# Performance work log

Hardware: AMD Instinct MI355X
Metric: run time of the kernel (lower is better)

## Reference

```python
import jax, jax.numpy as jnp
import numpy as np

NUM_GROUPS = 4
NUM_HEADS = 8
EPS = 1e-5


def setup_inputs() -> dict:
    key = jax.random.key(0)
    k1, k2, k3 = jax.random.split(key, 3)
    B, C, D, H, W = 4, 256, 32, 32, 32
    x = jax.random.normal(k1, (B, C, D, H, W), dtype=jnp.float32)
    gn_weight = jnp.ones((C,), dtype=jnp.float32)
    gn_bias = jnp.zeros((C,), dtype=jnp.float32)
    # 1x1x1 conv weights collapse to [out_ch, in_ch] matrices
    qkv_weight = jax.random.normal(k2, (3 * C, C), dtype=jnp.float32) * (1.0 / np.sqrt(C))
    out_weight = jax.random.normal(k3, (C, C), dtype=jnp.float32) * (1.0 / np.sqrt(C))
    out_bias = jnp.zeros((C,), dtype=jnp.float32)
    return {"x": x, "gn_weight": gn_weight, "gn_bias": gn_bias,
            "qkv_weight": qkv_weight, "out_weight": out_weight, "out_bias": out_bias}


def _group_norm(x, weight, bias):
    B, C, D, H, W = x.shape
    g = NUM_GROUPS
    xg = x.reshape(B, g, C // g, D, H, W)
    mean = jnp.mean(xg, axis=(2, 3, 4, 5), keepdims=True)
    var = jnp.var(xg, axis=(2, 3, 4, 5), keepdims=True)
    xn = ((xg - mean) * jax.lax.rsqrt(var + EPS)).reshape(B, C, D, H, W)
    return xn * weight[None, :, None, None, None] + bias[None, :, None, None, None]


def reference(x, gn_weight, gn_bias, qkv_weight, out_weight, out_bias):
    B, C, D, H, W = x.shape
    N = D * H * W
    hd = C // NUM_HEADS  # per-head channels

    norm = _group_norm(x, gn_weight, gn_bias)
    # 1x1x1 conv == channel matmul: [B,3C,D,H,W]
    qkv = jnp.einsum('bcdhw,oc->bodhw', norm, qkv_weight)
    # 'b (qkv heads c) d h w -> qkv b heads c (d h w)'
    qkv = qkv.reshape(B, 3, NUM_HEADS, hd, N)
    q, k, v = qkv[:, 0], qkv[:, 1], qkv[:, 2]  # each [B, heads, hd, N]

    k = jax.nn.softmax(k, axis=-1)  # softmax over spatial dim
    sim = jnp.einsum('bhdn,bhen->bhde', k, v)   # [B, heads, hd, hd]
    out = jnp.einsum('bhde,bhdn->bhen', sim, q)  # [B, heads, hd, N]
    out = out.reshape(B, C, D, H, W)

    out = jnp.einsum('bcdhw,oc->bodhw', out, out_weight) + out_bias[None, :, None, None, None]
    return out + x
```

## Files before the change

### kernel.cpp

```cpp
#include <hip/hip_runtime.h>
#include <cmath>


typedef __bf16 bf16x8 __attribute__((ext_vector_type(8)));
typedef float f32x4 __attribute__((ext_vector_type(4)));

union U16 { uint4 u; unsigned short s[8]; bf16x8 v; };

__device__ __forceinline__ float bf2f(unsigned short h) {
    unsigned int u = ((unsigned int)h) << 16;
    return __builtin_bit_cast(float, u);
}
__device__ __forceinline__ unsigned short f2bf(float f) {
    unsigned int u = __builtin_bit_cast(unsigned int, f);
    u = (u + 0x7fffu + ((u >> 16) & 1u)) >> 16;
    return (unsigned short)u;
}
__device__ __forceinline__ unsigned int pack2(unsigned short a, unsigned short b) {
    return (unsigned int)a | ((unsigned int)b << 16);
}

__global__ __launch_bounds__(64) void k_detect(const unsigned int* __restrict__ xr,
                                               int* __restrict__ flag) {
    unsigned int u = xr[threadIdx.x * 997];
    int e = (u >> 7) & 0xFF;
    bool ok = (e >= 100) && (e <= 141);
    unsigned long long m = __ballot(ok);
    if (threadIdx.x == 0) *flag = (__popcll(m) < 32) ? 1 : 0;
}

__global__ __launch_bounds__(256) void k_cvt_w(const void* __restrict__ qkvw,
                                               const void* __restrict__ outw,
                                               const void* __restrict__ gnw,
                                               const void* __restrict__ gnb,
                                               const void* __restrict__ outb,
                                               const int* __restrict__ flagp,
                                               unsigned short* __restrict__ wdst) {
    int idx = blockIdx.x * 256 + threadIdx.x;
    if (idx >= 262912) return;
    const void* src; int off;
    if      (idx < 196608) { src = qkvw; off = idx; }
    else if (idx < 262144) { src = outw; off = idx - 196608; }
    else if (idx < 262400) { src = gnw;  off = idx - 262144; }
    else if (idx < 262656) { src = gnb;  off = idx - 262400; }
    else                   { src = outb; off = idx - 262656; }
    int f = *flagp;
    wdst[idx] = f ? f2bf(((const float*)src)[off])
                  : ((const unsigned short*)src)[off];
}

__global__ __launch_bounds__(256) void k_cvt_x(const void* __restrict__ xr,
                                               const int* __restrict__ flagp,
                                               unsigned short* __restrict__ xw) {
    int f = *flagp;
    size_t base = ((size_t)blockIdx.x * 256 + threadIdx.x) * 8;
    if (f) {
        const float* xf = (const float*)xr;
        float4 a = *(const float4*)(xf + base);
        float4 c = *(const float4*)(xf + base + 4);
        U16 o;
        o.s[0] = f2bf(a.x); o.s[1] = f2bf(a.y); o.s[2] = f2bf(a.z); o.s[3] = f2bf(a.w);
        o.s[4] = f2bf(c.x); o.s[5] = f2bf(c.y); o.s[6] = f2bf(c.z); o.s[7] = f2bf(c.w);
        *(uint4*)(xw + base) = o.u;
    } else {
        *(uint4*)(xw + base) = *(const uint4*)((const unsigned short*)xr + base);
    }
}

__global__ __launch_bounds__(256) void k_gnsum(const unsigned short* __restrict__ x,
                                               float2* __restrict__ gn_part) {
    int t = threadIdx.x, bid = blockIdx.x;
    int grp = bid >> 7, chunk = bid & 127;
    const unsigned short* p = x + (size_t)grp * 2097152 + (size_t)chunk * 16384;
    float s = 0.f, q = 0.f;
    for (int i = 0; i < 8; i++) {
        U16 u; u.u = *(const uint4*)(p + i * 2048 + t * 8);
#pragma unroll
        for (int j = 0; j < 8; j++) { float f = bf2f(u.s[j]); s += f; q += f * f; }
    }
#pragma unroll
    for (int off = 32; off > 0; off >>= 1) { s += __shfl_xor(s, off); q += __shfl_xor(q, off); }
    __shared__ float rs[4], rq[4];
    int wave = t >> 6;
    if ((t & 63) == 0) { rs[wave] = s; rq[wave] = q; }
    __syncthreads();
    if (t == 0) gn_part[bid] = make_float2(rs[0] + rs[1] + rs[2] + rs[3],
                                           rq[0] + rq[1] + rq[2] + rq[3]);
}

__global__ __launch_bounds__(128) void k_gnfinal(const float2* __restrict__ gn_part,
                                                 float2* __restrict__ gstats) {
    int bg = blockIdx.x, t = threadIdx.x;
    float2 v = gn_part[bg * 128 + t];
    float s = v.x, q = v.y;
#pragma unroll
    for (int off = 32; off > 0; off >>= 1) { s += __shfl_xor(s, off); q += __shfl_xor(q, off); }
    __shared__ float rs[2], rq[2];
    if ((t & 63) == 0) { rs[t >> 6] = s; rq[t >> 6] = q; }
    __syncthreads();
    if (t == 0) {
        const float inv = 1.0f / 2097152.0f;
        float S = rs[0] + rs[1], Q = rq[0] + rq[1];
        float mean = S * inv;
        float var = Q * inv - mean * mean;
        gstats[bg] = make_float2(mean, rsqrtf(var + 1e-5f));
    }
}

__global__ __launch_bounds__(64) void k_beta(const unsigned short* __restrict__ wq,
                                             const unsigned short* __restrict__ wgnw,
                                             const unsigned short* __restrict__ wgnb,
                                             const float2* __restrict__ gstats,
                                             float* __restrict__ beta) {
    int bid = blockIdx.x;
    int b = bid / 768, o = bid % 768;
    int t = threadIdx.x, c = t * 4;
    float2 ms = gstats[b * 4 + (c >> 6)];
    uint2 qw = *(const uint2*)(wq + o * 256 + c);
    uint2 gw = *(const uint2*)(wgnw + c);
    uint2 gb = *(const uint2*)(wgnb + c);
    unsigned short qs[4] = {(unsigned short)(qw.x & 0xffff), (unsigned short)(qw.x >> 16),
                            (unsigned short)(qw.y & 0xffff), (unsigned short)(qw.y >> 16)};
    unsigned short wsx[4] = {(unsigned short)(gw.x & 0xffff), (unsigned short)(gw.x >> 16),
                             (unsigned short)(gw.y & 0xffff), (unsigned short)(gw.y >> 16)};
    unsigned short bs[4] = {(unsigned short)(gb.x & 0xffff), (unsigned short)(gb.x >> 16),
                            (unsigned short)(gb.y & 0xffff), (unsigned short)(gb.y >> 16)};
    float bacc = 0.f;
#pragma unroll
    for (int j = 0; j < 4; j++)
        bacc += bf2f(qs[j]) * (bf2f(bs[j]) - ms.x * ms.y * bf2f(wsx[j]));
#pragma unroll
    for (int off = 32; off > 0; off >>= 1) bacc += __shfl_xor(bacc, off);
    if (t == 0) beta[b * 768 + o] = bacc;
}

__global__ __launch_bounds__(256) void k_transpose(const unsigned short* __restrict__ x,
                                                   const unsigned short* __restrict__ wgnw,
                                                   const float2* __restrict__ gstats,
                                                   unsigned short* __restrict__ xt) {
    int tid = threadIdx.x, bid = blockIdx.x;
    int b = bid >> 11, r2 = bid & 2047, cblk = r2 >> 9, nblk = r2 & 511;
    float rstd = gstats[b * 4 + cblk].y;
    __shared__ __align__(16) unsigned short T[64 * 80];
    unsigned short tmp[2][8];
#pragma unroll
    for (int i = 0; i < 2; i++) {
        int crow = (tid >> 3) + 32 * i, nch = tid & 7;
        int c = cblk * 64 + crow;
        float sc = bf2f(wgnw[c]) * rstd;
        U16 u; u.u = *(const uint4*)(x + ((size_t)(b * 256 + c)) * 32768 + (size_t)nblk * 64 + nch * 8);
#pragma unroll
        for (int j = 0; j < 8; j++) tmp[i][j] = f2bf(bf2f(u.s[j]) * sc);
    }
#pragma unroll
    for (int i = 0; i < 2; i++) {
        int crow = (tid >> 3) + 32 * i, nch = tid & 7;
#pragma unroll
        for (int jj = 0; jj < 8; jj++) {
            int j = (jj + tid) & 7;
            T[(nch * 8 + j) * 80 + crow] = tmp[i][j];
        }
    }
    __syncthreads();
#pragma unroll
    for (int i = 0; i < 2; i++) {
        int nrow = (tid >> 3) + 32 * i, cch = tid & 7;
        uint4 v = *(const uint4*)&T[nrow * 80 + cch * 8];
        *(uint4*)(xt + ((size_t)b * 32768 + (size_t)nblk * 64 + nrow) * 256 + cblk * 64 + cch * 8) = v;
    }
}

__device__ __forceinline__ void stage128x64(const unsigned short* __restrict__ g,
                                            unsigned short* __restrict__ lds, int tid) {
    int wave = tid >> 6;
    int lane = tid & 63;
    const unsigned short* gl = g + (size_t)(lane >> 3) * 256 + (lane & 7) * 8;
    uint4 v[4];
#pragma unroll
    for (int i = 0; i < 4; i++)
        v[i] = *(const uint4*)(gl + (size_t)(wave * 32 + i * 8) * 256);
#pragma unroll
    for (int i = 0; i < 4; i++) {
        int row = wave * 32 + i * 8 + (lane >> 3);
        *(uint4*)&lds[row * 64 + (lane & 7) * 8] = v[i];
    }
}

__device__ __forceinline__ void gemm_core(const unsigned short* __restrict__ A,
                                          const unsigned short* __restrict__ Bsrc,
                                          unsigned short* ldsA, unsigned short* ldsB,
                                          int tid, f32x4 (&acc)[4][4]) {
    int lane = tid & 63, l15 = lane & 15, quad = lane >> 4;
    int wave = tid >> 6, wm = wave & 1, wn = wave >> 1;
    for (int kt = 0; kt < 4; kt++) {
        stage128x64(A + kt * 64, ldsA, tid);
        stage128x64(Bsrc + kt * 64, ldsB, tid);
        __syncthreads();
#pragma unroll
        for (int ks = 0; ks < 2; ks++) {
            bf16x8 af[4], bv[4];
#pragma unroll
            for (int mi = 0; mi < 4; mi++)
                af[mi] = *(const bf16x8*)&ldsA[(wm * 64 + mi * 16 + l15) * 64 + ks * 32 + quad * 8];
#pragma unroll
            for (int ni = 0; ni < 4; ni++)
                bv[ni] = *(const bf16x8*)&ldsB[(wn * 64 + ni * 16 + l15) * 64 + ks * 32 + quad * 8];
#pragma unroll
            for (int mi = 0; mi < 4; mi++)
#pragma unroll
                for (int ni = 0; ni < 4; ni++)
                    acc[mi][ni] = __builtin_amdgcn_mfma_f32_16x16x32_bf16(af[mi], bv[ni], acc[mi][ni], 0, 0, 0);
        }
        __syncthreads();
    }
}

__global__ __launch_bounds__(256) void k_gemm1(const unsigned short* __restrict__ wq,
                                               const unsigned short* __restrict__ xt,
                                               const float* __restrict__ beta,
                                               unsigned short* __restrict__ qT,
                                               unsigned short* __restrict__ kv) {
    __shared__ __align__(16) unsigned short ldsA[128 * 64];
    __shared__ __align__(16) unsigned short ldsB[128 * 64];
    int tid = threadIdx.x, bid = blockIdx.x;
    int b = bid / 1536, r = bid % 1536, mblk = r >> 8, nblk = r & 255;
    int o0 = mblk * 128;
    size_t n0 = (size_t)nblk * 128;
    const unsigned short* A = wq + (size_t)o0 * 256;
    const unsigned short* Bx = xt + ((size_t)b * 32768 + n0) * 256;
    f32x4 acc[4][4] = {};
    gemm_core(A, Bx, ldsA, ldsB, tid, acc);

    int lane = tid & 63, l15 = lane & 15, quad = lane >> 4;
    int wave = tid >> 6, wm = wave & 1, wn = wave >> 1;
    bool isQ = (mblk < 2);
#pragma unroll
    for (int mi = 0; mi < 4; mi++) {
        int o = o0 + wm * 64 + mi * 16 + quad * 4;
        float4 be = *(const float4*)(beta + b * 768 + o);
#pragma unroll
        for (int ni = 0; ni < 4; ni++) {
            size_t n = n0 + wn * 64 + ni * 16 + l15;
            f32x4 v = acc[mi][ni];
            unsigned short h0 = f2bf(v[0] + be.x), h1 = f2bf(v[1] + be.y);
            unsigned short h2 = f2bf(v[2] + be.z), h3 = f2bf(v[3] + be.w);
            if (isQ) {
                uint2 pv; pv.x = pack2(h0, h1); pv.y = pack2(h2, h3);
                *(uint2*)(qT + ((size_t)b * 32768 + n) * 256 + o) = pv;
            } else {
                int kvi = o - 256;
                unsigned short* bp = kv + ((size_t)b * 512 + kvi) * 32768 + n;
                bp[0] = h0; bp[32768] = h1; bp[65536] = h2; bp[98304] = h3;
            }
        }
    }
}

__global__ __launch_bounds__(256) void k_stats(const unsigned short* __restrict__ kv,
                                               float2* __restrict__ stats) {
    int row = blockIdx.x, t = threadIdx.x;
    const unsigned short* p = kv + ((size_t)(row >> 8) * 512 + (row & 255)) * 32768;
    float m = -3.0e38f;
    for (int i = 0; i < 16; i++) {
        U16 u; u.u = *(const uint4*)(p + i * 2048 + t * 8);
#pragma unroll
        for (int j = 0; j < 8; j++) m = fmaxf(m, bf2f(u.s[j]));
    }
#pragma unroll
    for (int off = 32; off > 0; off >>= 1) m = fmaxf(m, __shfl_xor(m, off));
    __shared__ float rm[4], rs[4];
    int wave = t >> 6;
    if ((t & 63) == 0) rm[wave] = m;
    __syncthreads();
    m = fmaxf(fmaxf(rm[0], rm[1]), fmaxf(rm[2], rm[3]));
    float s = 0.f;
    for (int i = 0; i < 16; i++) {
        U16 u; u.u = *(const uint4*)(p + i * 2048 + t * 8);
#pragma unroll
        for (int j = 0; j < 8; j++) s += __expf(bf2f(u.s[j]) - m);
    }
#pragma unroll
    for (int off = 32; off > 0; off >>= 1) s += __shfl_xor(s, off);
    if ((t & 63) == 0) rs[wave] = s;
    __syncthreads();
    if (t == 0) stats[row] = make_float2(m, 1.0f / (rs[0] + rs[1] + rs[2] + rs[3]));
}

__global__ __launch_bounds__(64) void k_sim(const unsigned short* __restrict__ kv,
                                            const float2* __restrict__ stats,
                                            float* __restrict__ partials) {
    int bid = blockIdx.x;
    int bh = bid >> 6, chunk = bid & 63;
    int b = bh >> 3, h = bh & 7;
    int lane = threadIdx.x, l15 = lane & 15, quad = lane >> 4;
    size_t n0 = (size_t)chunk * 512 + quad * 8;
    float mrow[2], isr[2];
#pragma unroll
    for (int mi = 0; mi < 2; mi++) {
        float2 st = stats[b * 256 + h * 32 + mi * 16 + l15];
        mrow[mi] = st.x; isr[mi] = st.y;
    }
    const unsigned short* kb = kv + ((size_t)b * 512 + h * 32) * 32768;
    const unsigned short* vb = kv + ((size_t)b * 512 + 256 + h * 32) * 32768;
    f32x4 acc[2][2] = {};
    for (int t = 0; t < 16; t++) {
        size_t n = n0 + t * 32;
        bf16x8 af[2], bv[2];
#pragma unroll
        for (int mi = 0; mi < 2; mi++) {
            U16 u; u.u = *(const uint4*)(kb + (size_t)(mi * 16 + l15) * 32768 + n);
            U16 pv;
#pragma unroll
            for (int j = 0; j < 8; j++) pv.s[j] = f2bf(__expf(bf2f(u.s[j]) - mrow[mi]) * isr[mi]);
            af[mi] = pv.v;
        }
#pragma unroll
        for (int ni = 0; ni < 2; ni++) {
            U16 u; u.u = *(const uint4*)(vb + (size_t)(ni * 16 + l15) * 32768 + n);
            bv[ni] = u.v;
        }
#pragma unroll
        for (int mi = 0; mi < 2; mi++)
#pragma unroll
            for (int ni = 0; ni < 2; ni++)
                acc[mi][ni] = __builtin_amdgcn_mfma_f32_16x16x32_bf16(af[mi], bv[ni], acc[mi][ni], 0, 0, 0);
    }
    float* po = partials + (size_t)(bh * 64 + chunk) * 1024;
#pragma unroll
    for (int mi = 0; mi < 2; mi++)
#pragma unroll
        for (int ni = 0; ni < 2; ni++)
#pragma unroll
            for (int rr = 0; rr < 4; rr++)
                po[(mi * 16 + quad * 4 + rr) * 32 + ni * 16 + l15] = acc[mi][ni][rr];
}

__global__ __launch_bounds__(256) void k_combine(const float* __restrict__ partials,
                                                 float* __restrict__ sim) {
    int bh = blockIdx.x, tid = threadIdx.x;
#pragma unroll
    for (int i = 0; i < 4; i++) {
        float a = 0.f;
        const float* p = partials + (size_t)bh * 65536 + tid + i * 256;
        for (int c = 0; c < 64; c++) a += p[(size_t)c * 1024];
        sim[bh * 1024 + tid + i * 256] = a;
    }
}

__global__ __launch_bounds__(256) void k_buildM(const unsigned short* __restrict__ wo,
                                                const float* __restrict__ sim,
                                                unsigned short* __restrict__ M) {
    int bid = blockIdx.x, tid = threadIdx.x;
    int b = bid >> 8, o = bid & 255;
    __shared__ float lw[256];
    __shared__ float ls[8192];
    lw[tid] = bf2f(wo[o * 256 + tid]);
#pragma unroll
    for (int i = 0; i < 32; i++) ls[tid + i * 256] = sim[(size_t)b * 8192 + tid + i * 256];
    __syncthreads();
    int h = tid >> 5, d = tid & 31;
    float a = 0.f;
#pragma unroll
    for (int e = 0; e < 32; e++) {
        int ee = (e + d) & 31;
        a += lw[h * 32 + ee] * ls[h * 1024 + d * 32 + ee];
    }
    M[((size_t)b * 256 + o) * 256 + tid] = f2bf(a);
}

__global__ __launch_bounds__(256) void k_gemm2(const unsigned short* __restrict__ qT,
                                               const unsigned short* __restrict__ M,
                                               const unsigned short* __restrict__ wob,
                                               const void* __restrict__ xr,
                                               const int* __restrict__ flagp,
                                               void* __restrict__ outv,
                                               int b0) {
    __shared__ __align__(16) unsigned short ldsA[128 * 64];
    __shared__ __align__(16) unsigned short ldsB[128 * 64];
    int tid = threadIdx.x, bid = blockIdx.x;
    int b = bid >> 9, r = bid & 511, oblk = r >> 8, mblk = r & 255;
    size_t n0 = (size_t)mblk * 128;
    int o0 = oblk * 128;
    const unsigned short* A = qT + ((size_t)b * 32768 + n0) * 256;
    const unsigned short* Bm = M + ((size_t)b * 256 + o0) * 256;
    f32x4 acc[4][4] = {};
    gemm_core(A, Bm, ldsA, ldsB, tid, acc);

    int f = *flagp;
    int gb = b0 + b;
    int lane = tid & 63, l15 = lane & 15, quad = lane >> 4;
    int wave = tid >> 6, wm = wave & 1, wn = wave >> 1;
#pragma unroll
    for (int mi = 0; mi < 4; mi++) {
        size_t n = n0 + wm * 64 + mi * 16 + quad * 4;
#pragma unroll
        for (int ni = 0; ni < 4; ni++) {
            int o = o0 + wn * 64 + ni * 16 + l15;
            float bias = bf2f(wob[o]);
            size_t base = ((size_t)gb * 256 + o) * 32768 + n;
            f32x4 v = acc[mi][ni];
            if (f) {
                float4 xv = *(const float4*)((const float*)xr + base);
                float4 ov = make_float4(v[0] + bias + xv.x, v[1] + bias + xv.y,
                                        v[2] + bias + xv.z, v[3] + bias + xv.w);
                *(float4*)((float*)outv + base) = ov;
            } else {
                uint2 xr2 = *(const uint2*)((const unsigned short*)xr + base);
                unsigned short xs[4] = {(unsigned short)(xr2.x & 0xffff), (unsigned short)(xr2.x >> 16),
                                        (unsigned short)(xr2.y & 0xffff), (unsigned short)(xr2.y >> 16)};
                uint2 pv;
                pv.x = pack2(f2bf(v[0] + bias + bf2f(xs[0])), f2bf(v[1] + bias + bf2f(xs[1])));
                pv.y = pack2(f2bf(v[2] + bias + bf2f(xs[2])), f2bf(v[3] + bias + bf2f(xs[3])));
                *(uint2*)((unsigned short*)outv + base) = pv;
            }
        }
    }
}

extern "C" void kernel_launch(void* const* d_in, const int* in_sizes, int n_in,
                              void* d_out, int out_size, void* d_ws, size_t ws_size,
                              hipStream_t stream) {
    const void* x    = d_in[0];
    const void* gnw  = d_in[1];
    const void* gnb  = d_in[2];
    const void* qkvw = d_in[3];
    const void* outw = d_in[4];
    const void* outb = d_in[5];
    char* ws = (char*)d_ws;

    unsigned short* xw    = (unsigned short*)(ws);
    unsigned short* wdst  = (unsigned short*)(ws + 67108864);
    int*            flag  = (int*)(ws + 68157440);
    float2*         gstats= (float2*)(ws + 68157456);
    float*          beta  = (float*)(ws + 68158464);
    float2*         stats = (float2*)(ws + 68174848);
    const size_t passbase = 69206016;

    const unsigned short* wq   = wdst;
    const unsigned short* wo   = wdst + 196608;
    const unsigned short* wgnw = wdst + 262144;
    const unsigned short* wgnb = wdst + 262400;
    const unsigned short* wob  = wdst + 262656;

    int nb;
    if      (ws_size >= passbase + 4ull * 67108864) nb = 4;
    else if (ws_size >= passbase + 2ull * 67108864) nb = 2;
    else                                            nb = 1;

    size_t qT_off = passbase;
    size_t kv_off = passbase + (size_t)nb * 16777216;
    size_t xt_off = kv_off + (size_t)nb * 33554432;

    unsigned short* qT = (unsigned short*)(ws + qT_off);
    unsigned short* kv = (unsigned short*)(ws + kv_off);
    unsigned short* xt = (unsigned short*)(ws + xt_off);
    float2* gn_part    = (float2*)(ws + kv_off);
    unsigned short* M  = (unsigned short*)(ws + kv_off);
    float* partials    = (float*)(ws + xt_off);
    float* sim         = (float*)(ws + xt_off + (size_t)nb * 2097152);

    k_detect<<<dim3(1), dim3(64), 0, stream>>>((const unsigned int*)x, flag);
    k_cvt_w<<<dim3(1027), dim3(256), 0, stream>>>(qkvw, outw, gnw, gnb, outb, flag, wdst);
    k_cvt_x<<<dim3(16384), dim3(256), 0, stream>>>(x, flag, xw);

    for (int pass = 0; pass < 4; pass += nb) {
        const unsigned short* xp = xw + (size_t)pass * 8388608;
        k_gnsum    <<<dim3(512 * nb),  dim3(256), 0, stream>>>(xp, gn_part);
        k_gnfinal  <<<dim3(4 * nb),    dim3(128), 0, stream>>>(gn_part, gstats);
        k_beta     <<<dim3(768 * nb),  dim3(64),  0, stream>>>(wq, wgnw, wgnb, gstats, beta);
        k_transpose<<<dim3(2048 * nb), dim3(256), 0, stream>>>(xp, wgnw, gstats, xt);
        k_gemm1    <<<dim3(1536 * nb), dim3(256), 0, stream>>>(wq, xt, beta, qT, kv);
        k_stats    <<<dim3(256 * nb),  dim3(256), 0, stream>>>(kv, stats);
        k_sim      <<<dim3(512 * nb),  dim3(64),  0, stream>>>(kv, stats, partials);
        k_combine  <<<dim3(8 * nb),    dim3(256), 0, stream>>>(partials, sim);
        k_buildM   <<<dim3(256 * nb),  dim3(256), 0, stream>>>(wo, sim, M);
        k_gemm2    <<<dim3(512 * nb),  dim3(256), 0, stream>>>(qT, M, wob, x, flag, d_out, pass);
    }
}
```

Baseline: 561.8 us.

## Swizzle GEMM LDS tiles, remap blocks, and stage epilogue stores through LDS

XOR-swizzles the LDS layout of the A/B tiles in the shared GEMM core to avoid bank conflicts on the MFMA fragment loads. Remaps block IDs across 8 groups so neighbouring blocks share operands, for better L2 locality. Rewrites the epilogues of both GEMMs to transpose results through LDS so that global stores (q, kv, and the fp32 output with residual) become coalesced 16-byte rows instead of scattered 2-byte or strided writes. This adds extra LDS traffic and barriers in the epilogues.

```diff
diff --git a/kernel.cpp b/kernel.cpp
--- a/kernel.cpp
+++ b/kernel.cpp
@@ -174,15 +174,19 @@
                                             unsigned short* __restrict__ lds, int tid) {
     int wave = tid >> 6;
     int lane = tid & 63;
-    const unsigned short* gl = g + (size_t)(lane >> 3) * 256 + (lane & 7) * 8;
+    int rsub = lane >> 3;
+    int slot = lane & 7;
     uint4 v[4];
 #pragma unroll
-    for (int i = 0; i < 4; i++)
-        v[i] = *(const uint4*)(gl + (size_t)(wave * 32 + i * 8) * 256);
-#pragma unroll
     for (int i = 0; i < 4; i++) {
-        int row = wave * 32 + i * 8 + (lane >> 3);
-        *(uint4*)&lds[row * 64 + (lane & 7) * 8] = v[i];
+        int row = wave * 32 + i * 8 + rsub;
+        v[i] = *(const uint4*)(g + (size_t)row * 256 + slot * 8);
+    }
+#pragma unroll
+    for (int i = 0; i < 4; i++) {
+        int row = wave * 32 + i * 8 + rsub;
+        int s = slot ^ (row & 7);
+        *(uint4*)&lds[row * 64 + s * 8] = v[i];
     }
 }
 
@@ -200,11 +204,15 @@
         for (int ks = 0; ks < 2; ks++) {
             bf16x8 af[4], bv[4];
 #pragma unroll
-            for (int mi = 0; mi < 4; mi++)
-                af[mi] = *(const bf16x8*)&ldsA[(wm * 64 + mi * 16 + l15) * 64 + ks * 32 + quad * 8];
-#pragma unroll
-            for (int ni = 0; ni < 4; ni++)
-                bv[ni] = *(const bf16x8*)&ldsB[(wn * 64 + ni * 16 + l15) * 64 + ks * 32 + quad * 8];
+            for (int mi = 0; mi < 4; mi++) {
+                int row = wm * 64 + mi * 16 + l15;
+                af[mi] = *(const bf16x8*)&ldsA[row * 64 + (((ks * 4 + quad) ^ (row & 7)) * 8)];
+            }
+#pragma unroll
+            for (int ni = 0; ni < 4; ni++) {
+                int row = wn * 64 + ni * 16 + l15;
+                bv[ni] = *(const bf16x8*)&ldsB[row * 64 + (((ks * 4 + quad) ^ (row & 7)) * 8)];
+            }
 #pragma unroll
             for (int mi = 0; mi < 4; mi++)
 #pragma unroll
@@ -220,10 +228,14 @@
                                                const float* __restrict__ beta,
                                                unsigned short* __restrict__ qT,
                                                unsigned short* __restrict__ kv) {
-    __shared__ __align__(16) unsigned short ldsA[128 * 64];
-    __shared__ __align__(16) unsigned short ldsB[128 * 64];
+    __shared__ __align__(16) unsigned short ldsbuf[2 * 128 * 64];
+    unsigned short* ldsA = ldsbuf;
+    unsigned short* ldsB = ldsbuf + 128 * 64;
     int tid = threadIdx.x, bid = blockIdx.x;
-    int b = bid / 1536, r = bid % 1536, mblk = r >> 8, nblk = r & 255;
+    int L = (bid & 7) * ((int)gridDim.x >> 3) + (bid >> 3);
+    int mblk = L % 6;
+    int t2 = L / 6;
+    int nblk = t2 & 255, b = t2 >> 8;
     int o0 = mblk * 128;
     size_t n0 = (size_t)nblk * 128;
     const unsigned short* A = wq + (size_t)o0 * 256;
@@ -234,24 +246,54 @@
     int lane = tid & 63, l15 = lane & 15, quad = lane >> 4;
     int wave = tid >> 6, wm = wave & 1, wn = wave >> 1;
     bool isQ = (mblk < 2);
-#pragma unroll
-    for (int mi = 0; mi < 4; mi++) {
-        int o = o0 + wm * 64 + mi * 16 + quad * 4;
-        float4 be = *(const float4*)(beta + b * 768 + o);
-#pragma unroll
-        for (int ni = 0; ni < 4; ni++) {
-            size_t n = n0 + wn * 64 + ni * 16 + l15;
-            f32x4 v = acc[mi][ni];
-            unsigned short h0 = f2bf(v[0] + be.x), h1 = f2bf(v[1] + be.y);
-            unsigned short h2 = f2bf(v[2] + be.z), h3 = f2bf(v[3] + be.w);
-            if (isQ) {
-                uint2 pv; pv.x = pack2(h0, h1); pv.y = pack2(h2, h3);
-                *(uint2*)(qT + ((size_t)b * 32768 + n) * 256 + o) = pv;
-            } else {
-                int kvi = o - 256;
-                unsigned short* bp = kv + ((size_t)b * 512 + kvi) * 32768 + n;
-                bp[0] = h0; bp[32768] = h1; bp[65536] = h2; bp[98304] = h3;
+    if (isQ) {
+#pragma unroll
+        for (int mi = 0; mi < 4; mi++) {
+            int o_l = wm * 64 + mi * 16 + quad * 4;
+            float4 be = *(const float4*)(beta + b * 768 + o0 + o_l);
+#pragma unroll
+            for (int ni = 0; ni < 4; ni++) {
+                int n_l = wn * 64 + ni * 16 + l15;
+                f32x4 v = acc[mi][ni];
+                uint2 pv;
+                pv.x = pack2(f2bf(v[0] + be.x), f2bf(v[1] + be.y));
+                pv.y = pack2(f2bf(v[2] + be.z), f2bf(v[3] + be.w));
+                *(uint2*)&ldsbuf[(n_l * 128 + o_l) ^ ((n_l & 7) << 3)] = pv;
             }
+        }
+        __syncthreads();
+#pragma unroll
+        for (int p = 0; p < 8; p++) {
+            int n_l = p * 16 + (tid >> 4);
+            int ch = tid & 15;
+            uint4 v = *(const uint4*)&ldsbuf[(n_l * 128 + ch * 8) ^ ((n_l & 7) << 3)];
+            *(uint4*)(qT + ((size_t)b * 32768 + n0 + n_l) * 256 + o0 + ch * 8) = v;
+        }
+    } else {
+#pragma unroll
+        for (int mi = 0; mi < 4; mi++) {
+            int o_l = wm * 64 + mi * 16 + quad * 4;
+            float4 be = *(const float4*)(beta + b * 768 + o0 + o_l);
+            float bev[4] = {be.x, be.y, be.z, be.w};
+#pragma unroll
+            for (int ni = 0; ni < 4; ni++) {
+                int n_l = wn * 64 + ni * 16 + l15;
+                f32x4 v = acc[mi][ni];
+#pragma unroll
+                for (int r = 0; r < 4; r++) {
+                    int o_r = o_l + r;
+                    ldsbuf[(o_r * 128 + n_l) ^ ((o_r & 7) << 3)] = f2bf(v[r] + bev[r]);
+                }
+            }
+        }
+        __syncthreads();
+        int kv0 = o0 - 256;
+#pragma unroll
+        for (int p = 0; p < 8; p++) {
+            int o_r = p * 16 + (tid >> 4);
+            int ch = tid & 15;
+            uint4 v = *(const uint4*)&ldsbuf[(o_r * 128 + ch * 8) ^ ((o_r & 7) << 3)];
+            *(uint4*)(kv + ((size_t)b * 512 + kv0 + o_r) * 32768 + n0 + ch * 8) = v;
         }
     }
 }
@@ -375,10 +417,15 @@
                                                const int* __restrict__ flagp,
                                                void* __restrict__ outv,
                                                int b0) {
-    __shared__ __align__(16) unsigned short ldsA[128 * 64];
-    __shared__ __align__(16) unsigned short ldsB[128 * 64];
+    __shared__ __align__(16) unsigned short ldsbuf[2 * 128 * 64];
+    unsigned short* ldsA = ldsbuf;
+    unsigned short* ldsB = ldsbuf + 128 * 64;
+    float* ldsF = (float*)ldsbuf;
     int tid = threadIdx.x, bid = blockIdx.x;
-    int b = bid >> 9, r = bid & 511, oblk = r >> 8, mblk = r & 255;
+    int L = (bid & 7) * ((int)gridDim.x >> 3) + (bid >> 3);
+    int oblk = L & 1;
+    int t2 = L >> 1;
+    int mblk = t2 & 255, b = t2 >> 8;
     size_t n0 = (size_t)mblk * 128;
     int o0 = oblk * 128;
     const unsigned short* A = qT + ((size_t)b * 32768 + n0) * 256;
@@ -390,30 +437,47 @@
     int gb = b0 + b;
     int lane = tid & 63, l15 = lane & 15, quad = lane >> 4;
     int wave = tid >> 6, wm = wave & 1, wn = wave >> 1;
-#pragma unroll
-    for (int mi = 0; mi < 4; mi++) {
-        size_t n = n0 + wm * 64 + mi * 16 + quad * 4;
-#pragma unroll
-        for (int ni = 0; ni < 4; ni++) {
-            int o = o0 + wn * 64 + ni * 16 + l15;
+    for (int half = 0; half < 2; half++) {
+        if (wn == half) {
+#pragma unroll
+            for (int mi = 0; mi < 4; mi++) {
+#pragma unroll
+                for (int ni = 0; ni < 4; ni++) {
+                    int o_h = ni * 16 + l15;
+                    f32x4 v = acc[mi][ni];
+#pragma unroll
+                    for (int r = 0; r < 4; r++) {
+                        int n_l = wm * 64 + mi * 16 + quad * 4 + r;
+                        ldsF[(o_h * 128 + n_l) ^ ((o_h & 15) << 2)] = v[r];
+                    }
+                }
+            }
+        }
+        __syncthreads();
+#pragma unroll
+        for (int p = 0; p < 8; p++) {
+            int o_h = p * 8 + (tid >> 5);
+            int ch = tid & 31;
+            float4 v = *(const float4*)&ldsF[(o_h * 128 + ch * 4) ^ ((o_h & 15) << 2)];
+            int o = o0 + half * 64 + o_h;
             float bias = bf2f(wob[o]);
-            size_t base = ((size_t)gb * 256 + o) * 32768 + n;
-            f32x4 v = acc[mi][ni];
+            size_t base = ((size_t)gb * 256 + o) * 32768 + n0 + ch * 4;
             if (f) {
                 float4 xv = *(const float4*)((const float*)xr + base);
-                float4 ov = make_float4(v[0] + bias + xv.x, v[1] + bias + xv.y,
-                                        v[2] + bias + xv.z, v[3] + bias + xv.w);
+                float4 ov = make_float4(v.x + bias + xv.x, v.y + bias + xv.y,
+                                        v.z + bias + xv.z, v.w + bias + xv.w);
                 *(float4*)((float*)outv + base) = ov;
             } else {
                 uint2 xr2 = *(const uint2*)((const unsigned short*)xr + base);
                 unsigned short xs[4] = {(unsigned short)(xr2.x & 0xffff), (unsigned short)(xr2.x >> 16),
                                         (unsigned short)(xr2.y & 0xffff), (unsigned short)(xr2.y >> 16)};
                 uint2 pv;
-                pv.x = pack2(f2bf(v[0] + bias + bf2f(xs[0])), f2bf(v[1] + bias + bf2f(xs[1])));
-                pv.y = pack2(f2bf(v[2] + bias + bf2f(xs[2])), f2bf(v[3] + bias + bf2f(xs[3])));
+                pv.x = pack2(f2bf(v.x + bias + bf2f(xs[0])), f2bf(v.y + bias + bf2f(xs[1])));
+                pv.y = pack2(f2bf(v.z + bias + bf2f(xs[2])), f2bf(v.w + bias + bf2f(xs[3])));
                 *(uint2*)((unsigned short*)outv + base) = pv;
             }
         }
+        __syncthreads();
     }
 }
 
```

Result: slower. 591.5 us (+5.3%).
